# Optimization experiments

Measured on AMD Instinct MI355X. Metric: run time of the kernel, lower is better.

The kernel has to match this reference:

```python
import jax, jax.numpy as jnp
import numpy as np
from jax import lax

H = 50  # hidden size of every LSTM layer


def _lstm_layer(x, w_ih, w_hh, b_ih, b_hh):
    """PyTorch-semantics LSTM (gate order i,f,g,o), zero initial state.
    x: [B,T,D] -> returns hidden sequence [B,T,H]."""
    # Precompute input contribution for all timesteps (one big GEMM).
    xw = jnp.einsum('btd,gd->btg', x, w_ih) + (b_ih + b_hh)  # [B,T,4H]
    xw = jnp.transpose(xw, (1, 0, 2))  # time-major [T,B,4H]

    def step(carry, xt):
        h, c = carry
        gates = xt + h @ w_hh.T  # [B,4H]
        i, f, g, o = jnp.split(gates, 4, axis=-1)
        i = jax.nn.sigmoid(i)
        f = jax.nn.sigmoid(f)
        g = jnp.tanh(g)
        o = jax.nn.sigmoid(o)
        c = f * c + i * g
        h = o * jnp.tanh(c)
        return (h, c), h

    B = x.shape[0]
    h0 = jnp.zeros((B, H), x.dtype)
    c0 = jnp.zeros((B, H), x.dtype)
    _, hs = lax.scan(step, (h0, c0), xw)  # hs: [T,B,H]
    return jnp.transpose(hs, (1, 0, 2))


def setup_inputs() -> dict:
    key = jax.random.key(0)
    ks = jax.random.split(key, 15)
    B, T = 512, 1024
    s = 1.0 / np.sqrt(H)  # PyTorch default uniform(-1/sqrt(H), 1/sqrt(H))

    def u(k, shape):
        return jax.random.uniform(k, shape, jnp.float32, -s, s)

    inp = {
        'x': jax.random.normal(ks[0], (B, T, 1), jnp.float32),
        'w_ih1': u(ks[1], (4 * H, 1)),  'w_hh1': u(ks[2], (4 * H, H)),
        'b_ih1': u(ks[3], (4 * H,)),    'b_hh1': u(ks[4], (4 * H,)),
        'w_ih2': u(ks[5], (4 * H, H)),  'w_hh2': u(ks[6], (4 * H, H)),
        'b_ih2': u(ks[7], (4 * H,)),    'b_hh2': u(ks[8], (4 * H,)),
        'w_ih3': u(ks[9], (4 * H, H)),  'w_hh3': u(ks[10], (4 * H, H)),
        'b_ih3': u(ks[11], (4 * H,)),   'b_hh3': u(ks[12], (4 * H,)),
        'w_dense': u(ks[13], (1, H)),   'b_dense': u(ks[14], (1,)),
    }
    return inp


def reference(x, w_ih1, w_hh1, b_ih1, b_hh1,
              w_ih2, w_hh2, b_ih2, b_hh2,
              w_ih3, w_hh3, b_ih3, b_hh3,
              w_dense, b_dense):
    h = _lstm_layer(x, w_ih1, w_hh1, b_ih1, b_hh1)
    h = _lstm_layer(h, w_ih2, w_hh2, b_ih2, b_hh2)
    h = _lstm_layer(h, w_ih3, w_hh3, b_ih3, b_hh3)
    last = h[:, -1, :]  # [B,H]
    return last @ w_dense.T + b_dense  # [B,1]
```

## Files before the change

kernel.cpp:

```cpp
#include <hip/hip_runtime.h>
#include <hip/hip_bf16.h>
#include <cstddef>

#define H    50
#define G4   200
#define TT   1024
#define BB   512
#define BLK  512

__device__ __forceinline__ float sigm(float x) { return 1.0f / (1.0f + __expf(-x)); }
__device__ __forceinline__ float tanh_fast(float x) { return 1.0f - 2.0f / (__expf(2.0f * x) + 1.0f); }

#define BAR() do { asm volatile("s_waitcnt lgkmcnt(0)" ::: "memory"); \
                   __builtin_amdgcn_s_barrier(); } while (0)

#define D13(P) float P##0,P##1,P##2,P##3,P##4,P##5,P##6,P##7,P##8,P##9,P##10,P##11,P##12

#define WL13(P, WPTR, ROW, K0) do { const float* _w = (WPTR) + (size_t)(ROW) * H; const int _k = (K0); \
  P##0 =(_k+ 0<H)?_w[_k+ 0]:0.f; P##1 =(_k+ 1<H)?_w[_k+ 1]:0.f; P##2 =(_k+ 2<H)?_w[_k+ 2]:0.f; \
  P##3 =(_k+ 3<H)?_w[_k+ 3]:0.f; P##4 =(_k+ 4<H)?_w[_k+ 4]:0.f; P##5 =(_k+ 5<H)?_w[_k+ 5]:0.f; \
  P##6 =(_k+ 6<H)?_w[_k+ 6]:0.f; P##7 =(_k+ 7<H)?_w[_k+ 7]:0.f; P##8 =(_k+ 8<H)?_w[_k+ 8]:0.f; \
  P##9 =(_k+ 9<H)?_w[_k+ 9]:0.f; P##10=(_k+10<H)?_w[_k+10]:0.f; P##11=(_k+11<H)?_w[_k+11]:0.f; \
  P##12=(_k+12<H)?_w[_k+12]:0.f; } while (0)

#define HT13(P, HS, K0) float P##0=(HS)[(K0)+0], P##1=(HS)[(K0)+1], P##2 =(HS)[(K0)+2], \
  P##3=(HS)[(K0)+3], P##4=(HS)[(K0)+4],  P##5 =(HS)[(K0)+5],  P##6 =(HS)[(K0)+6], \
  P##7=(HS)[(K0)+7], P##8=(HS)[(K0)+8],  P##9 =(HS)[(K0)+9],  P##10=(HS)[(K0)+10], \
  P##11=(HS)[(K0)+11], P##12=(HS)[(K0)+12]

#define DOT13(W, X, A) do { \
  A=__fmaf_rn(W##0,X##0,A);  A=__fmaf_rn(W##1,X##1,A);  A=__fmaf_rn(W##2,X##2,A); \
  A=__fmaf_rn(W##3,X##3,A);  A=__fmaf_rn(W##4,X##4,A);  A=__fmaf_rn(W##5,X##5,A); \
  A=__fmaf_rn(W##6,X##6,A);  A=__fmaf_rn(W##7,X##7,A);  A=__fmaf_rn(W##8,X##8,A); \
  A=__fmaf_rn(W##9,X##9,A);  A=__fmaf_rn(W##10,X##10,A); A=__fmaf_rn(W##11,X##11,A); \
  A=__fmaf_rn(W##12,X##12,A); } while (0)

#define XL13(P, BASE) do { const size_t _b = (BASE); \
  P##0 = xrow[_b];                          P##1 =(k0x+ 1<H)?xrow[_b+ 1]:xrow[_b]; \
  P##2 =(k0x+ 2<H)?xrow[_b+ 2]:xrow[_b];    P##3 =(k0x+ 3<H)?xrow[_b+ 3]:xrow[_b]; \
  P##4 =(k0x+ 4<H)?xrow[_b+ 4]:xrow[_b];    P##5 =(k0x+ 5<H)?xrow[_b+ 5]:xrow[_b]; \
  P##6 =(k0x+ 6<H)?xrow[_b+ 6]:xrow[_b];    P##7 =(k0x+ 7<H)?xrow[_b+ 7]:xrow[_b]; \
  P##8 =(k0x+ 8<H)?xrow[_b+ 8]:xrow[_b];    P##9 =(k0x+ 9<H)?xrow[_b+ 9]:xrow[_b]; \
  P##10=(k0x+10<H)?xrow[_b+10]:xrow[_b];    P##11=(k0x+11<H)?xrow[_b+11]:xrow[_b]; \
  P##12=(k0x+12<H)?xrow[_b+12]:xrow[_b]; } while (0)

#define XCOMP(SRC, NB) do { float _p0=0.f,_p1=0.f,_p2=0.f,_p3=0.f; \
  DOT13(wA,SRC,_p0); DOT13(wB,SRC,_p1); DOT13(wC,SRC,_p2); DOT13(wD,SRC,_p3); \
  xw_s[NB][0][ux][qx]=_p0; xw_s[NB][1][ux][qx]=_p1; \
  xw_s[NB][2][ux][qx]=_p2; xw_s[NB][3][ux][qx]=_p3; } while (0)

#define STEP(CUR, T, XSRC, XDST) do { \
  if (hw) { \
    HT13(ht, h_s[CUR], k0h); \
    float a0=0.f, a1=0.f, a2=0.f, a3=0.f; \
    DOT13(wA, ht, a0); DOT13(wB, ht, a1); DOT13(wC, ht, a2); DOT13(wD, ht, a3); \
    if (MODE != 0) { \
      a0 += xw_s[CUR][0][uh][qh]; a1 += xw_s[CUR][1][uh][qh]; \
      a2 += xw_s[CUR][2][uh][qh]; a3 += xw_s[CUR][3][uh][qh]; \
    } \
    a0 += __shfl_xor(a0, 1); a0 += __shfl_xor(a0, 2); \
    a1 += __shfl_xor(a1, 1); a1 += __shfl_xor(a1, 2); \
    a2 += __shfl_xor(a2, 1); a2 += __shfl_xor(a2, 2); \
    a3 += __shfl_xor(a3, 1); a3 += __shfl_xor(a3, 2); \
    if (MODE == 0) { float _xt = x_s[T]; \
      a0 = __fmaf_rn(wi0,_xt,a0); a1 = __fmaf_rn(wi1,_xt,a1); \
      a2 = __fmaf_rn(wi2,_xt,a2); a3 = __fmaf_rn(wi3,_xt,a3); } \
    float iv = sigm(a0 + bb0), fv = sigm(a1 + bb1); \
    float gv = tanh_fast(a2 + bb2), ov = sigm(a3 + bb3); \
    c_r  = __fmaf_rn(fv, c_r, iv * gv); \
    hval = ov * tanh_fast(c_r); \
    if (hvalid) { \
      h_s[(CUR)^1][uh] = hval; \
      if (MODE != 2) hout[hob + (size_t)(T) * H + uh] = hval; \
    } \
  } else if (MODE != 0) { \
    if ((T) + 2 < TT) { XL13(XDST, (size_t)((T)+2) * H + k0x); } \
    if ((T) + 1 < TT) { XCOMP(XSRC, (CUR)^1); } \
  } \
  BAR(); \
} while (0)

template <int MODE>
__global__ __launch_bounds__(BLK, 4) __attribute__((amdgpu_waves_per_eu(4, 4)))
void lstm_kernel(
    const float* __restrict__ xin,
    const float* __restrict__ w_ih,
    const float* __restrict__ w_hh,
    const float* __restrict__ b_ih,
    const float* __restrict__ b_hh,
    float* __restrict__ hout,
    const float* __restrict__ w_dense,
    const float* __restrict__ b_dense,
    float* __restrict__ out)
{
    const int b   = blockIdx.x;
    const int tid = threadIdx.x;
    const int wv  = tid >> 6;
    const int ln  = tid & 63;
    const bool hw = (wv < 4);

    const int uh  = (wv & 3) * 16 + (ln >> 2);
    const int qh  = ln & 3;
    const int k0h = 13 * qh;
    const int uch = (uh < H) ? uh : (H - 1);
    const bool hvalid = hw && (uh < H) && (qh == 0);

    const int ux  = uh, qx = qh, k0x = k0h, ucx = uch;

    __shared__ float h_s[2][52];
    __shared__ float xw_s[2][4][64][4];
    __shared__ float x_s[MODE == 0 ? TT : 1];

    D13(wA); D13(wB); D13(wC); D13(wD);
    D13(xa); D13(xb);
    float wi0 = 0.f, wi1 = 0.f, wi2 = 0.f, wi3 = 0.f;
    float bb0 = 0.f, bb1 = 0.f, bb2 = 0.f, bb3 = 0.f;

    const float* __restrict__ xrow = xin + (size_t)b * TT * (MODE == 0 ? 1 : H);
    const size_t hob = (size_t)b * TT * H;

    if (hw) {
        WL13(wA, w_hh, 0 * H + uch, k0h);
        WL13(wB, w_hh, 1 * H + uch, k0h);
        WL13(wC, w_hh, 2 * H + uch, k0h);
        WL13(wD, w_hh, 3 * H + uch, k0h);
        bb0 = b_ih[0 * H + uch] + b_hh[0 * H + uch];
        bb1 = b_ih[1 * H + uch] + b_hh[1 * H + uch];
        bb2 = b_ih[2 * H + uch] + b_hh[2 * H + uch];
        bb3 = b_ih[3 * H + uch] + b_hh[3 * H + uch];
        if (MODE == 0) {
            wi0 = w_ih[0 * H + uch]; wi1 = w_ih[1 * H + uch];
            wi2 = w_ih[2 * H + uch]; wi3 = w_ih[3 * H + uch];
        }
    } else if (MODE != 0) {
        WL13(wA, w_ih, 0 * H + ucx, k0x);
        WL13(wB, w_ih, 1 * H + ucx, k0x);
        WL13(wC, w_ih, 2 * H + ucx, k0x);
        WL13(wD, w_ih, 3 * H + ucx, k0x);
    }
    float wdr = 0.f;
    if (MODE == 2 && wv == 0 && ln < H) wdr = w_dense[ln];

    if (tid < 104) (&h_s[0][0])[tid] = 0.f;
    if (MODE == 0) {
        for (int i = tid; i < TT; i += BLK) x_s[i] = xrow[i];
    } else if (!hw) {
        XL13(xb, (size_t)0 * H + k0x);
        XCOMP(xb, 0);
        XL13(xa, (size_t)1 * H + k0x);
    }
    float c_r = 0.f, hval = 0.f;
    __syncthreads();

    for (int t = 0; t < TT; t += 2) {
        STEP(0, t,     xa, xb);
        STEP(1, t + 1, xb, xa);
    }

    if (MODE == 2 && wv == 0) {
        float v = (ln < H) ? h_s[0][ln] * wdr : 0.f;
#pragma unroll
        for (int off = 32; off > 0; off >>= 1) v += __shfl_down(v, off, 64);
        if (ln == 0) out[b] = v + b_dense[0];
    }
}

extern "C" void kernel_launch(void* const* d_in, const int* in_sizes, int n_in,
                              void* d_out, int out_size, void* d_ws, size_t ws_size,
                              hipStream_t stream) {
    const float* x     = (const float*)d_in[0];
    const float* wih1  = (const float*)d_in[1];
    const float* whh1  = (const float*)d_in[2];
    const float* bih1  = (const float*)d_in[3];
    const float* bhh1  = (const float*)d_in[4];
    const float* wih2  = (const float*)d_in[5];
    const float* whh2  = (const float*)d_in[6];
    const float* bih2  = (const float*)d_in[7];
    const float* bhh2  = (const float*)d_in[8];
    const float* wih3  = (const float*)d_in[9];
    const float* whh3  = (const float*)d_in[10];
    const float* bih3  = (const float*)d_in[11];
    const float* bhh3  = (const float*)d_in[12];
    const float* wd    = (const float*)d_in[13];
    const float* bd    = (const float*)d_in[14];
    float* outp = (float*)d_out;
    float* hbuf = (float*)d_ws;

    lstm_kernel<0><<<BB, BLK, 0, stream>>>(x,    wih1, whh1, bih1, bhh1, hbuf, nullptr, nullptr, nullptr);
    lstm_kernel<1><<<BB, BLK, 0, stream>>>(hbuf, wih2, whh2, bih2, bhh2, hbuf, nullptr, nullptr, nullptr);
    lstm_kernel<2><<<BB, BLK, 0, stream>>>(hbuf, wih3, whh3, bih3, bhh3, nullptr, wd, bd, outp);
}
```

Before: 2.293 ms.

## Vectorize LDS slices, use DPP quad reductions, stage x input through LDS

The hidden state and input rows now live in padded 4x16 LDS slices, so each quad lane reads its 13-element chunk with three float4 loads plus one scalar instead of 13 scalar LDS reads. The xw tile is reordered so the four gate partials are written and read as one float4. The shfl_xor quad reductions are replaced with DPP row-permute adds. For layers 2 and 3, the input-projection waves no longer each load 13 global values per step. A single wave instead prefetches one row into a register and writes it into a double-buffered LDS slice, which the other waves then read. This aims to cut LDS instruction count and global load traffic on the per-step critical path, at the cost of more intricate buffer indexing and zero-padding invariants.

```diff
diff --git a/kernel.cpp b/kernel.cpp
--- a/kernel.cpp
+++ b/kernel.cpp
@@ -9,10 +9,17 @@
 #define BLK  512
 
 __device__ __forceinline__ float sigm(float x) { return 1.0f / (1.0f + __expf(-x)); }
-__device__ __forceinline__ float tanh_fast(float x) { return 1.0f - 2.0f / (__expf(2.0f * x) + 1.0f); }
+__device__ __forceinline__ float tanh_fast(float x){ return 1.0f - 2.0f / (__expf(2.0f*x) + 1.0f); }
 
 #define BAR() do { asm volatile("s_waitcnt lgkmcnt(0)" ::: "memory"); \
                    __builtin_amdgcn_s_barrier(); } while (0)
+
+#define QSUM(v) do { \
+  int _d = __builtin_amdgcn_mov_dpp(__float_as_int(v), 0xB1, 0xF, 0xF, true); \
+  (v) += __int_as_float(_d); \
+  _d = __builtin_amdgcn_mov_dpp(__float_as_int(v), 0x4E, 0xF, 0xF, true); \
+  (v) += __int_as_float(_d); \
+} while (0)
 
 #define D13(P) float P##0,P##1,P##2,P##3,P##4,P##5,P##6,P##7,P##8,P##9,P##10,P##11,P##12
 
@@ -23,59 +30,55 @@
   P##9 =(_k+ 9<H)?_w[_k+ 9]:0.f; P##10=(_k+10<H)?_w[_k+10]:0.f; P##11=(_k+11<H)?_w[_k+11]:0.f; \
   P##12=(_k+12<H)?_w[_k+12]:0.f; } while (0)
 
-#define HT13(P, HS, K0) float P##0=(HS)[(K0)+0], P##1=(HS)[(K0)+1], P##2 =(HS)[(K0)+2], \
-  P##3=(HS)[(K0)+3], P##4=(HS)[(K0)+4],  P##5 =(HS)[(K0)+5],  P##6 =(HS)[(K0)+6], \
-  P##7=(HS)[(K0)+7], P##8=(HS)[(K0)+8],  P##9 =(HS)[(K0)+9],  P##10=(HS)[(K0)+10], \
-  P##11=(HS)[(K0)+11], P##12=(HS)[(K0)+12]
-
-#define DOT13(W, X, A) do { \
-  A=__fmaf_rn(W##0,X##0,A);  A=__fmaf_rn(W##1,X##1,A);  A=__fmaf_rn(W##2,X##2,A); \
-  A=__fmaf_rn(W##3,X##3,A);  A=__fmaf_rn(W##4,X##4,A);  A=__fmaf_rn(W##5,X##5,A); \
-  A=__fmaf_rn(W##6,X##6,A);  A=__fmaf_rn(W##7,X##7,A);  A=__fmaf_rn(W##8,X##8,A); \
-  A=__fmaf_rn(W##9,X##9,A);  A=__fmaf_rn(W##10,X##10,A); A=__fmaf_rn(W##11,X##11,A); \
-  A=__fmaf_rn(W##12,X##12,A); } while (0)
-
-#define XL13(P, BASE) do { const size_t _b = (BASE); \
-  P##0 = xrow[_b];                          P##1 =(k0x+ 1<H)?xrow[_b+ 1]:xrow[_b]; \
-  P##2 =(k0x+ 2<H)?xrow[_b+ 2]:xrow[_b];    P##3 =(k0x+ 3<H)?xrow[_b+ 3]:xrow[_b]; \
-  P##4 =(k0x+ 4<H)?xrow[_b+ 4]:xrow[_b];    P##5 =(k0x+ 5<H)?xrow[_b+ 5]:xrow[_b]; \
-  P##6 =(k0x+ 6<H)?xrow[_b+ 6]:xrow[_b];    P##7 =(k0x+ 7<H)?xrow[_b+ 7]:xrow[_b]; \
-  P##8 =(k0x+ 8<H)?xrow[_b+ 8]:xrow[_b];    P##9 =(k0x+ 9<H)?xrow[_b+ 9]:xrow[_b]; \
-  P##10=(k0x+10<H)?xrow[_b+10]:xrow[_b];    P##11=(k0x+11<H)?xrow[_b+11]:xrow[_b]; \
-  P##12=(k0x+12<H)?xrow[_b+12]:xrow[_b]; } while (0)
-
-#define XCOMP(SRC, NB) do { float _p0=0.f,_p1=0.f,_p2=0.f,_p3=0.f; \
-  DOT13(wA,SRC,_p0); DOT13(wB,SRC,_p1); DOT13(wC,SRC,_p2); DOT13(wD,SRC,_p3); \
-  xw_s[NB][0][ux][qx]=_p0; xw_s[NB][1][ux][qx]=_p1; \
-  xw_s[NB][2][ux][qx]=_p2; xw_s[NB][3][ux][qx]=_p3; } while (0)
-
-#define STEP(CUR, T, XSRC, XDST) do { \
+#define LDSLICE(A4, B4, C4, S1, BASE) do { \
+  const float4* _p = (const float4*)(BASE); \
+  A4 = _p[0]; B4 = _p[1]; C4 = _p[2]; S1 = ((const float*)(BASE))[12]; } while (0)
+
+#define DOT13Q(W, A4, B4, C4, S1, ACC) do { \
+  ACC=__fmaf_rn(W##0, (A4).x,ACC); ACC=__fmaf_rn(W##1, (A4).y,ACC); \
+  ACC=__fmaf_rn(W##2, (A4).z,ACC); ACC=__fmaf_rn(W##3, (A4).w,ACC); \
+  ACC=__fmaf_rn(W##4, (B4).x,ACC); ACC=__fmaf_rn(W##5, (B4).y,ACC); \
+  ACC=__fmaf_rn(W##6, (B4).z,ACC); ACC=__fmaf_rn(W##7, (B4).w,ACC); \
+  ACC=__fmaf_rn(W##8, (C4).x,ACC); ACC=__fmaf_rn(W##9, (C4).y,ACC); \
+  ACC=__fmaf_rn(W##10,(C4).z,ACC); ACC=__fmaf_rn(W##11,(C4).w,ACC); \
+  ACC=__fmaf_rn(W##12,(S1),  ACC); } while (0)
+
+#define STEP(CUR, T) do { \
   if (hw) { \
-    HT13(ht, h_s[CUR], k0h); \
-    float a0=0.f, a1=0.f, a2=0.f, a3=0.f; \
-    DOT13(wA, ht, a0); DOT13(wB, ht, a1); DOT13(wC, ht, a2); DOT13(wD, ht, a3); \
+    float4 hA,hB,hC; float h12; \
+    LDSLICE(hA,hB,hC,h12, &h_s[CUR][qh][0]); \
+    float a0=0.f,a1=0.f,a2=0.f,a3=0.f; \
+    DOT13Q(wA,hA,hB,hC,h12,a0); DOT13Q(wB,hA,hB,hC,h12,a1); \
+    DOT13Q(wC,hA,hB,hC,h12,a2); DOT13Q(wD,hA,hB,hC,h12,a3); \
     if (MODE != 0) { \
-      a0 += xw_s[CUR][0][uh][qh]; a1 += xw_s[CUR][1][uh][qh]; \
-      a2 += xw_s[CUR][2][uh][qh]; a3 += xw_s[CUR][3][uh][qh]; \
+      const float4 xw4 = *(const float4*)&xw_s[CUR][uh][qh][0]; \
+      a0 += xw4.x; a1 += xw4.y; a2 += xw4.z; a3 += xw4.w; \
     } \
-    a0 += __shfl_xor(a0, 1); a0 += __shfl_xor(a0, 2); \
-    a1 += __shfl_xor(a1, 1); a1 += __shfl_xor(a1, 2); \
-    a2 += __shfl_xor(a2, 1); a2 += __shfl_xor(a2, 2); \
-    a3 += __shfl_xor(a3, 1); a3 += __shfl_xor(a3, 2); \
+    QSUM(a0); QSUM(a1); QSUM(a2); QSUM(a3); \
     if (MODE == 0) { float _xt = x_s[T]; \
-      a0 = __fmaf_rn(wi0,_xt,a0); a1 = __fmaf_rn(wi1,_xt,a1); \
-      a2 = __fmaf_rn(wi2,_xt,a2); a3 = __fmaf_rn(wi3,_xt,a3); } \
+      a0=__fmaf_rn(wi0,_xt,a0); a1=__fmaf_rn(wi1,_xt,a1); \
+      a2=__fmaf_rn(wi2,_xt,a2); a3=__fmaf_rn(wi3,_xt,a3); } \
     float iv = sigm(a0 + bb0), fv = sigm(a1 + bb1); \
     float gv = tanh_fast(a2 + bb2), ov = sigm(a3 + bb3); \
     c_r  = __fmaf_rn(fv, c_r, iv * gv); \
     hval = ov * tanh_fast(c_r); \
     if (hvalid) { \
-      h_s[(CUR)^1][uh] = hval; \
+      h_s[(CUR)^1][slcw][idxw] = hval; \
       if (MODE != 2) hout[hob + (size_t)(T) * H + uh] = hval; \
     } \
   } else if (MODE != 0) { \
-    if ((T) + 2 < TT) { XL13(XDST, (size_t)((T)+2) * H + k0x); } \
-    if ((T) + 1 < TT) { XCOMP(XSRC, (CUR)^1); } \
+    if ((T) + 1 < TT) {  \
+      float4 xA,xB,xC; float x12; \
+      LDSLICE(xA,xB,xC,x12, &xls[((T)+1)&1][qh][0]); \
+      float p0=0.f,p1=0.f,p2=0.f,p3=0.f; \
+      DOT13Q(wA,xA,xB,xC,x12,p0); DOT13Q(wB,xA,xB,xC,x12,p1); \
+      DOT13Q(wC,xA,xB,xC,x12,p2); DOT13Q(wD,xA,xB,xC,x12,p3); \
+      *(float4*)&xw_s[(CUR)^1][uh][qh][0] = make_float4(p0,p1,p2,p3); \
+    } \
+    float r_next = 0.f; \
+    if (xio && (T) + 3 < TT) r_next = xrow[(size_t)((T)+3) * H + ln];  \
+    if (xio && (T) + 2 < TT) xls[(T)&1][slcx][idxx] = r_cur;           \
+    r_cur = r_next; \
   } \
   BAR(); \
 } while (0)
@@ -104,17 +107,18 @@
     const int k0h = 13 * qh;
     const int uch = (uh < H) ? uh : (H - 1);
     const bool hvalid = hw && (uh < H) && (qh == 0);
-
-    const int ux  = uh, qx = qh, k0x = k0h, ucx = uch;
-
-    __shared__ float h_s[2][52];
-    __shared__ float xw_s[2][4][64][4];
+    const int slcw = uch / 13, idxw = uch % 13;
+    const int slcx = (ln < H ? ln : 0) / 13, idxx = (ln < H ? ln : 0) % 13;
+    const bool xio = (MODE != 0) && (wv == 4) && (ln < H);
+
+    __shared__ __align__(16) float h_s[2][4][16];
+    __shared__ __align__(16) float xw_s[2][64][4][4];
+    __shared__ __align__(16) float xls[2][4][16];
     __shared__ float x_s[MODE == 0 ? TT : 1];
 
     D13(wA); D13(wB); D13(wC); D13(wD);
-    D13(xa); D13(xb);
-    float wi0 = 0.f, wi1 = 0.f, wi2 = 0.f, wi3 = 0.f;
-    float bb0 = 0.f, bb1 = 0.f, bb2 = 0.f, bb3 = 0.f;
+    float wi0=0.f, wi1=0.f, wi2=0.f, wi3=0.f;
+    float bb0=0.f, bb1=0.f, bb2=0.f, bb3=0.f;
 
     const float* __restrict__ xrow = xin + (size_t)b * TT * (MODE == 0 ? 1 : H);
     const size_t hob = (size_t)b * TT * H;
@@ -133,32 +137,45 @@
             wi2 = w_ih[2 * H + uch]; wi3 = w_ih[3 * H + uch];
         }
     } else if (MODE != 0) {
-        WL13(wA, w_ih, 0 * H + ucx, k0x);
-        WL13(wB, w_ih, 1 * H + ucx, k0x);
-        WL13(wC, w_ih, 2 * H + ucx, k0x);
-        WL13(wD, w_ih, 3 * H + ucx, k0x);
+        WL13(wA, w_ih, 0 * H + uch, k0h);
+        WL13(wB, w_ih, 1 * H + uch, k0h);
+        WL13(wC, w_ih, 2 * H + uch, k0h);
+        WL13(wD, w_ih, 3 * H + uch, k0h);
     }
     float wdr = 0.f;
     if (MODE == 2 && wv == 0 && ln < H) wdr = w_dense[ln];
 
-    if (tid < 104) (&h_s[0][0])[tid] = 0.f;
+    if (tid < 128) (&h_s[0][0][0])[tid] = 0.f;
+    if (tid >= 128 && tid < 132) {
+        int z = tid - 128; xls[z >> 1][3][11 + (z & 1)] = 0.f;
+    }
     if (MODE == 0) {
         for (int i = tid; i < TT; i += BLK) x_s[i] = xrow[i];
-    } else if (!hw) {
-        XL13(xb, (size_t)0 * H + k0x);
-        XCOMP(xb, 0);
-        XL13(xa, (size_t)1 * H + k0x);
-    }
+    } else if (xio) {
+        xls[0][slcx][idxx] = xrow[ln];
+        xls[1][slcx][idxx] = xrow[H + ln];
+    }
+    __syncthreads();
+    if (MODE != 0 && !hw) {
+        float4 xA,xB,xC; float x12;
+        LDSLICE(xA,xB,xC,x12, &xls[0][qh][0]);
+        float p0=0.f,p1=0.f,p2=0.f,p3=0.f;
+        DOT13Q(wA,xA,xB,xC,x12,p0); DOT13Q(wB,xA,xB,xC,x12,p1);
+        DOT13Q(wC,xA,xB,xC,x12,p2); DOT13Q(wD,xA,xB,xC,x12,p3);
+        *(float4*)&xw_s[0][uh][qh][0] = make_float4(p0,p1,p2,p3);
+    }
+    float r_cur = 0.f;
+    if (xio) r_cur = xrow[(size_t)2 * H + ln];
     float c_r = 0.f, hval = 0.f;
     __syncthreads();
 
     for (int t = 0; t < TT; t += 2) {
-        STEP(0, t,     xa, xb);
-        STEP(1, t + 1, xb, xa);
+        STEP(0, t);
+        STEP(1, t + 1);
     }
 
     if (MODE == 2 && wv == 0) {
-        float v = (ln < H) ? h_s[0][ln] * wdr : 0.f;
+        float v = (ln < H) ? h_s[0][ln / 13][ln % 13] * wdr : 0.f;
 #pragma unroll
         for (int off = 32; off > 0; off >>= 1) v += __shfl_down(v, off, 64);
         if (ln == 0) out[b] = v + b_dense[0];
```

Result: slower. 2.504 ms (+9.2%).
